# Optimization experiments

Hardware: AMD Instinct MI355X
Metric: run time of the kernel (lower is better)

Reference implementation:

```python
import jax, jax.numpy as jnp
import numpy as np

D_IN = 1024
D_OUT = 1024
NUM_HEADS = 16
HEAD_DIM = D_OUT // NUM_HEADS
WINDOW = 256


def setup_inputs() -> dict:
    key = jax.random.key(0)
    ks = jax.random.split(key, 6)
    s = 0.02
    x = jax.random.normal(ks[0], (2, 2048, D_IN), dtype=jnp.float32)
    Wq = jax.random.normal(ks[1], (D_IN, D_OUT), dtype=jnp.float32) * s
    Wk = jax.random.normal(ks[2], (D_IN, D_OUT), dtype=jnp.float32) * s
    Wv = jax.random.normal(ks[3], (D_IN, D_OUT), dtype=jnp.float32) * s
    Wo = jax.random.normal(ks[4], (D_OUT, D_OUT), dtype=jnp.float32) * s
    bo = jnp.zeros((D_OUT,), dtype=jnp.float32)
    return {"x": x, "Wq": Wq, "Wk": Wk, "Wv": Wv, "Wo": Wo, "bo": bo}


def reference(x, Wq, Wk, Wv, Wo, bo):
    b, s, _ = x.shape
    # project and split heads: [b, h, s, hd]
    def heads(t):
        return t.reshape(b, s, NUM_HEADS, HEAD_DIM).transpose(0, 2, 1, 3)
    q = heads(x @ Wq)
    k = heads(x @ Wk)
    v = heads(x @ Wv)
    scores = jnp.einsum('bhqd,bhkd->bhqk', q, k) / jnp.sqrt(jnp.float32(HEAD_DIM))
    # symmetric sliding-window band: |i - j| <= WINDOW
    i = jnp.arange(s)
    band = jnp.abs(i[:, None] - i[None, :]) <= WINDOW  # [s, s]
    scores = jnp.where(band[None, None], scores, -jnp.inf)
    probs = jax.nn.softmax(scores, axis=-1)  # dropout=0.0 -> identity
    ctx = jnp.einsum('bhqk,bhkd->bhqd', probs, v)
    ctx = ctx.transpose(0, 2, 1, 3).reshape(b, s, D_OUT)
    return ctx @ Wo + bo
```

## Files before the change

### kernel.cpp

```cpp
#include <hip/hip_runtime.h>
#include <hip/hip_bf16.h>

typedef __bf16 bf16_t;
typedef __bf16 bf16x8 __attribute__((ext_vector_type(8)));
typedef __bf16 bf16x4 __attribute__((ext_vector_type(4)));
typedef float  f32x4  __attribute__((ext_vector_type(4)));

#define SEQ    2048
#define BATCH  2
#define NHEAD  16
#define HDIM   64
#define DMODEL 1024
#define WIN    256

__device__ __forceinline__ void async_load16(const void* g, void* l) {
    __builtin_amdgcn_global_load_lds(
        (const __attribute__((address_space(1))) char*)(uintptr_t)g,
        (__attribute__((address_space(3))) char*)(uintptr_t)l, 16, 0, 0);
}

__global__ __launch_bounds__(256) void prep_kernel(
    const float* __restrict__ x, const float* __restrict__ Wq,
    const float* __restrict__ Wk, const float* __restrict__ Wv,
    const float* __restrict__ Wo, bf16_t* __restrict__ xb,
    bf16_t* __restrict__ Wt) {
    const int bid = blockIdx.x, tid = threadIdx.x;
    if (bid < 1024) {
        __shared__ float t64[64][65];
        const int mat = bid >> 8, tile = bid & 255;
        const int k0 = (tile >> 4) * 64, n0 = (tile & 15) * 64;
        const float* W = (mat == 0) ? Wq : (mat == 1) ? Wk : (mat == 2) ? Wv : Wo;
        bf16_t* out = Wt + (size_t)mat * DMODEL * DMODEL;
        const int r = tid >> 4, c4 = tid & 15;
#pragma unroll
        for (int i = 0; i < 4; i++) {
            int krow = i * 16 + r;
            float4 v = *(const float4*)&W[(size_t)(k0 + krow) * DMODEL + n0 + c4 * 4];
            t64[krow][c4 * 4 + 0] = v.x; t64[krow][c4 * 4 + 1] = v.y;
            t64[krow][c4 * 4 + 2] = v.z; t64[krow][c4 * 4 + 3] = v.w;
        }
        __syncthreads();
#pragma unroll
        for (int j = 0; j < 4; j++) {
            int nrow = j * 16 + r;
            bf16x4 o;
#pragma unroll
            for (int q = 0; q < 4; q++) o[q] = (bf16_t)t64[c4 * 4 + q][nrow];
            *(bf16x4*)&out[(size_t)(n0 + nrow) * DMODEL + k0 + c4 * 4] = o;
        }
    } else {
        const int cb = bid - 1024;
#pragma unroll
        for (int it = 0; it < 4; it++) {
            int i = (cb * 4 + it) * 256 + tid;
            float4 v = ((const float4*)x)[i];
            bf16x4 o;
            o[0] = (bf16_t)v.x; o[1] = (bf16_t)v.y; o[2] = (bf16_t)v.z; o[3] = (bf16_t)v.w;
            ((bf16x4*)xb)[i] = o;
        }
    }
}

__global__ __launch_bounds__(512) void gemm_qkv_kernel(
    const bf16_t* __restrict__ A, const bf16_t* __restrict__ Bt,
    bf16_t* __restrict__ Qb, bf16_t* __restrict__ Kb, bf16_t* __restrict__ Vt) {
    __shared__ __attribute__((aligned(16))) bf16_t smem[2][(256 + 192) * 64];
    const int tid = threadIdx.x;
    const int wave = tid >> 6, lane = tid & 63, quad = lane >> 4, l15 = lane & 15;
    const int wm = wave >> 2, wn = wave & 3;
    const int id = blockIdx.x, xcd = id & 7, tt = id >> 3;
    const int gidx = xcd * 32 + tt;
    const int m0 = (gidx & 15) * 256, n0 = (gidx >> 4) * 192;

    const int cth = (tid & 7) ^ ((tid >> 3) & 7);
    const int rA = tid >> 3;

    auto stage = [&](int tile, int buf) {
#pragma unroll
        for (int gr = 0; gr < 4; ++gr)
            async_load16(A + (size_t)(m0 + gr * 64 + rA) * 1024 + tile * 64 + cth * 8,
                         (char*)&smem[buf][0] + (size_t)(gr * 512 + tid) * 16);
#pragma unroll
        for (int gr = 0; gr < 3; ++gr)
            async_load16(Bt + (size_t)(n0 + gr * 64 + rA) * 1024 + tile * 64 + cth * 8,
                         (char*)&smem[buf][256 * 64] + (size_t)(gr * 512 + tid) * 16);
    };

    const int swz  = l15 & 7;
    const int rowA = wm * 128 + l15;
    const int rowB = wn * 48 + l15;

    f32x4 acc[8][3] = {};

    stage(0, 0);
    __syncthreads();
    int cur = 0;
#pragma unroll 1
    for (int t = 0; t < 16; ++t) {
        if (t + 1 < 16) stage(t + 1, cur ^ 1);
        const bf16_t* as = &smem[cur][0];
        const bf16_t* bs = &smem[cur][256 * 64];
#pragma unroll
        for (int kk = 0; kk < 2; ++kk) {
            const int chk = ((kk * 4 + quad) ^ swz) * 8;
            bf16x8 am[8], bn[3];
#pragma unroll
            for (int i = 0; i < 8; i++)
                am[i] = *(const bf16x8*)&as[(rowA + i * 16) * 64 + chk];
#pragma unroll
            for (int j = 0; j < 3; j++)
                bn[j] = *(const bf16x8*)&bs[(rowB + j * 16) * 64 + chk];
#pragma unroll
            for (int i = 0; i < 8; i++)
#pragma unroll
                for (int j = 0; j < 3; j++)
                    acc[i][j] = __builtin_amdgcn_mfma_f32_16x16x32_bf16(am[i], bn[j], acc[i][j], 0, 0, 0);
        }
        __syncthreads();
        cur ^= 1;
    }

#pragma unroll
    for (int i = 0; i < 8; i++)
#pragma unroll
        for (int j = 0; j < 3; j++) {
            const int mg0 = m0 + wm * 128 + i * 16 + quad * 4;
            const int ng  = n0 + wn * 48 + j * 16 + l15;
            const int sel = ng >> 10, nl = ng & 1023, h = nl >> 6, d = nl & 63;
            const int b = mg0 >> 11, s0 = mg0 & 2047;
            if (sel == 2) {
                bf16x4 o;
#pragma unroll
                for (int r = 0; r < 4; r++) o[r] = (bf16_t)acc[i][j][r];
                *(bf16x4*)&Vt[((size_t)((b * NHEAD + h) * HDIM + d)) * SEQ + s0] = o;
            } else {
#pragma unroll
                for (int r = 0; r < 4; r++) {
                    float v = acc[i][j][r];
                    size_t idx = ((size_t)((b * NHEAD + h) * SEQ) + s0 + r) * HDIM + d;
                    if (sel == 0) Qb[idx] = (bf16_t)(v * 0.18033688011112042f);
                    else          Kb[idx] = (bf16_t)v;
                }
            }
        }
}

__global__ __launch_bounds__(256) void gemm_out_kernel(
    const bf16_t* __restrict__ A, const bf16_t* __restrict__ Bt,
    float* __restrict__ Out, const float* __restrict__ bo) {
    __shared__ __attribute__((aligned(16))) bf16_t As[2][64 * 64];
    __shared__ __attribute__((aligned(16))) bf16_t Bs[2][128 * 64];
    const int tid = threadIdx.x;
    const int wn = tid >> 6, lane = tid & 63, quad = lane >> 4, l15 = lane & 15;
    const int id = blockIdx.x, xcd = id & 7, mt = id >> 3;
    const int m0 = mt * 64, n0 = xcd * 128;

    auto stage = [&](int kt, int buf) {
#pragma unroll
        for (int i = 0; i < 2; i++) {
            int v = tid + i * 256;
            int row = v >> 3, c = (v & 7) ^ (row & 7);
            async_load16(A + (size_t)(m0 + row) * 1024 + kt * 64 + c * 8,
                         (char*)&As[buf][0] + (size_t)v * 16);
        }
#pragma unroll
        for (int i = 0; i < 4; i++) {
            int v = tid + i * 256;
            int row = v >> 3, c = (v & 7) ^ (row & 7);
            async_load16(Bt + (size_t)(n0 + row) * 1024 + kt * 64 + c * 8,
                         (char*)&Bs[buf][0] + (size_t)v * 16);
        }
    };

    f32x4 acc[4][2] = {};
    stage(0, 0);
    __syncthreads();
    int cur = 0;
    for (int kt = 0; kt < 16; ++kt) {
        if (kt + 1 < 16) stage(kt + 1, cur ^ 1);
#pragma unroll
        for (int kk = 0; kk < 64; kk += 32) {
            bf16x8 am[4], bn[2];
#pragma unroll
            for (int i = 0; i < 4; i++) {
                int row = i * 16 + l15;
                int ch = ((kk >> 3) + quad) ^ (row & 7);
                am[i] = *(const bf16x8*)&As[cur][row * 64 + ch * 8];
            }
#pragma unroll
            for (int j = 0; j < 2; j++) {
                int row = wn * 32 + j * 16 + l15;
                int ch = ((kk >> 3) + quad) ^ (row & 7);
                bn[j] = *(const bf16x8*)&Bs[cur][row * 64 + ch * 8];
            }
#pragma unroll
            for (int i = 0; i < 4; i++)
#pragma unroll
                for (int j = 0; j < 2; j++)
                    acc[i][j] = __builtin_amdgcn_mfma_f32_16x16x32_bf16(am[i], bn[j], acc[i][j], 0, 0, 0);
        }
        __syncthreads();
        cur ^= 1;
    }

#pragma unroll
    for (int i = 0; i < 4; i++)
#pragma unroll
        for (int j = 0; j < 2; j++)
#pragma unroll
            for (int r = 0; r < 4; r++) {
                int mg = m0 + i * 16 + quad * 4 + r;
                int ng = n0 + wn * 32 + j * 16 + l15;
                Out[(size_t)mg * DMODEL + ng] = acc[i][j][r] + bo[ng];
            }
}

__global__ __launch_bounds__(512) void attn_kernel(
    const bf16_t* __restrict__ Qb, const bf16_t* __restrict__ Kb,
    const bf16_t* __restrict__ Vt, bf16_t* __restrict__ ctx) {
    __shared__ __attribute__((aligned(16))) bf16_t Ks[2][64 * 64];
    __shared__ __attribute__((aligned(16))) bf16_t Vs[2][64 * 64];
    __shared__ __attribute__((aligned(16))) bf16_t Plds[8][16][72];
    const int tid = threadIdx.x;
    const int wave = tid >> 6, lane = tid & 63, quad = lane >> 4, l15 = lane & 15;

    const int id = blockIdx.x;
    const int task = (id & 7) * 64 + (id >> 3);
    const int b = task >> 8, h = (task >> 4) & 15, Q0 = (task & 15) << 7;
    const int qbase = Q0 + wave * 16;
    const int wqt = (Q0 >> 6) + (wave >> 2);

    const bf16_t* Qp = Qb + (size_t)(b * NHEAD + h) * SEQ * HDIM;
    const bf16_t* Kp = Kb + (size_t)(b * NHEAD + h) * SEQ * HDIM;
    const bf16_t* Vp = Vt + (size_t)(b * NHEAD + h) * HDIM * SEQ;

    bf16x8 qa0 = *(const bf16x8*)(Qp + (size_t)(qbase + l15) * HDIM + quad * 8);
    bf16x8 qa1 = *(const bf16x8*)(Qp + (size_t)(qbase + l15) * HDIM + 32 + quad * 8);

    f32x4 O[4] = {};
    float psum = 0.0f;

    const int base_t = Q0 >> 6;
    const int bt0 = (base_t - 4 > 0) ? base_t - 4 : 0;
    const int bt1 = (base_t + 5 < SEQ / 64 - 1) ? base_t + 5 : SEQ / 64 - 1;

    auto stage = [&](int kt, int buf) {
        const int k0 = kt * 64;
        int v = tid;
        int row = v >> 3, c = (v & 7) ^ (row & 7);
        async_load16(Kp + (size_t)(k0 + row) * HDIM + c * 8, (char*)&Ks[buf][0] + (size_t)v * 16);
        async_load16(Vp + (size_t)row * SEQ + k0 + c * 8, (char*)&Vs[buf][0] + (size_t)v * 16);
    };

    stage(bt0, 0);
    int cb = 0;
    for (int kt = bt0; kt <= bt1; kt++) {
        __syncthreads();
        if (kt < bt1) stage(kt + 1, cb ^ 1);
        const int dt = kt - wqt;
        if (dt >= -4 && dt <= 4) {
            const int k0 = kt * 64;
            f32x4 st[4];
#pragma unroll
            for (int c = 0; c < 4; c++) {
                int row = c * 16 + l15;
                bf16x8 kb0 = *(const bf16x8*)&Ks[cb][row * 64 + (quad ^ (row & 7)) * 8];
                bf16x8 kb1 = *(const bf16x8*)&Ks[cb][row * 64 + ((quad + 4) ^ (row & 7)) * 8];
                f32x4 a = {};
                a = __builtin_amdgcn_mfma_f32_16x16x32_bf16(kb0, qa0, a, 0, 0, 0);
                a = __builtin_amdgcn_mfma_f32_16x16x32_bf16(kb1, qa1, a, 0, 0, 0);
                st[c] = a;
            }
            const bool edge = (dt == -4 || dt == 4);
            const int q = qbase + l15;
#pragma unroll
            for (int c = 0; c < 4; c++) {
                bf16x4 pk;
#pragma unroll
                for (int r = 0; r < 4; r++) {
                    float sv = st[c][r];
                    if (edge) {
                        int k = k0 + c * 16 + quad * 4 + r;
                        int dd = q - k; dd = (dd < 0) ? -dd : dd;
                        if (dd > WIN) sv = -1e30f;
                    }
                    pk[r] = (bf16_t)exp2f(sv);
                    psum += (float)pk[r];
                }
                *(bf16x4*)&Plds[wave][l15][c * 16 + quad * 4] = pk;
            }
            bf16x8 pa0 = *(const bf16x8*)&Plds[wave][l15][quad * 8];
            bf16x8 pa1 = *(const bf16x8*)&Plds[wave][l15][32 + quad * 8];
#pragma unroll
            for (int d = 0; d < 4; d++) {
                int row = d * 16 + l15;
                bf16x8 vb0 = *(const bf16x8*)&Vs[cb][row * 64 + (quad ^ (row & 7)) * 8];
                bf16x8 vb1 = *(const bf16x8*)&Vs[cb][row * 64 + ((quad + 4) ^ (row & 7)) * 8];
                O[d] = __builtin_amdgcn_mfma_f32_16x16x32_bf16(pa0, vb0, O[d], 0, 0, 0);
                O[d] = __builtin_amdgcn_mfma_f32_16x16x32_bf16(pa1, vb1, O[d], 0, 0, 0);
            }
        }
        cb ^= 1;
    }

    psum += __shfl_xor(psum, 16, 64);
    psum += __shfl_xor(psum, 32, 64);

#pragma unroll
    for (int r = 0; r < 4; r++) {
        float s_q = __shfl(psum, (quad << 4) | (quad * 4 + r), 64);
        float inv = 1.0f / s_q;
        int i = qbase + quad * 4 + r;
#pragma unroll
        for (int d = 0; d < 4; d++) {
            float v = O[d][r] * inv;
            ctx[((size_t)(b * SEQ + i)) * DMODEL + h * HDIM + d * 16 + l15] = (bf16_t)v;
        }
    }
}

extern "C" void kernel_launch(void* const* d_in, const int* in_sizes, int n_in,
                              void* d_out, int out_size, void* d_ws, size_t ws_size,
                              hipStream_t stream) {
    const float* x  = (const float*)d_in[0];
    const float* Wq = (const float*)d_in[1];
    const float* Wk = (const float*)d_in[2];
    const float* Wv = (const float*)d_in[3];
    const float* Wo = (const float*)d_in[4];
    const float* bo = (const float*)d_in[5];
    float* out = (float*)d_out;

    const size_t MTOK = (size_t)BATCH * SEQ;
    bf16_t* xb  = (bf16_t*)d_ws;
    bf16_t* Wt  = xb + MTOK * DMODEL;
    bf16_t* Qb  = Wt + (size_t)4 * DMODEL * DMODEL;
    bf16_t* Kb  = Qb + MTOK * DMODEL;
    bf16_t* Vt  = Kb + MTOK * DMODEL;
    bf16_t* ctx = Vt + MTOK * DMODEL;

    prep_kernel<<<dim3(2048), dim3(256), 0, stream>>>(x, Wq, Wk, Wv, Wo, xb, Wt);
    gemm_qkv_kernel<<<dim3(256), dim3(512), 0, stream>>>(xb, Wt, Qb, Kb, Vt);
    attn_kernel<<<dim3(512), dim3(512), 0, stream>>>(Qb, Kb, Vt, ctx);
    gemm_out_kernel<<<dim3(512), dim3(256), 0, stream>>>(
        ctx, Wt + (size_t)3 * DMODEL * DMODEL, out, bo);
}
```

Before: 156.9 us.

## Split attention KV range across wave halves with LDS merge of partial outputs

```diff
diff --git a/kernel.cpp b/kernel.cpp
--- a/kernel.cpp
+++ b/kernel.cpp
@@ -218,17 +218,22 @@
 __global__ __launch_bounds__(512) void attn_kernel(
     const bf16_t* __restrict__ Qb, const bf16_t* __restrict__ Kb,
     const bf16_t* __restrict__ Vt, bf16_t* __restrict__ ctx) {
-    __shared__ __attribute__((aligned(16))) bf16_t Ks[2][64 * 64];
-    __shared__ __attribute__((aligned(16))) bf16_t Vs[2][64 * 64];
-    __shared__ __attribute__((aligned(16))) bf16_t Plds[8][16][72];
+    __shared__ __attribute__((aligned(16))) char raw[51200];
+    bf16_t* Ks = (bf16_t*)&raw[0];
+    bf16_t* Vs = (bf16_t*)&raw[16384];
+    bf16_t (*Plds)[16][72] = (bf16_t(*)[16][72])&raw[32768];
+    float* Omrg = (float*)&raw[0];
+    float* Pmrg = (float*)&raw[16640];
+
     const int tid = threadIdx.x;
     const int wave = tid >> 6, lane = tid & 63, quad = lane >> 4, l15 = lane & 15;
+    const int p = wave & 3, half = wave >> 2;
 
     const int id = blockIdx.x;
-    const int task = (id & 7) * 64 + (id >> 3);
-    const int b = task >> 8, h = (task >> 4) & 15, Q0 = (task & 15) << 7;
-    const int qbase = Q0 + wave * 16;
-    const int wqt = (Q0 >> 6) + (wave >> 2);
+    const int task = (id & 7) * 128 + (id >> 3);
+    const int b = task >> 9, h = (task >> 5) & 15, Q0 = (task & 31) << 6;
+    const int qbase = Q0 + p * 16;
+    const int base_t = Q0 >> 6;
 
     const bf16_t* Qp = Qb + (size_t)(b * NHEAD + h) * SEQ * HDIM;
     const bf16_t* Kp = Kb + (size_t)(b * NHEAD + h) * SEQ * HDIM;
@@ -240,32 +245,37 @@
     f32x4 O[4] = {};
     float psum = 0.0f;
 
-    const int base_t = Q0 >> 6;
     const int bt0 = (base_t - 4 > 0) ? base_t - 4 : 0;
-    const int bt1 = (base_t + 5 < SEQ / 64 - 1) ? base_t + 5 : SEQ / 64 - 1;
+    const int bt1 = (base_t + 4 < SEQ / 64 - 1) ? base_t + 4 : SEQ / 64 - 1;
 
     auto stage = [&](int kt, int buf) {
         const int k0 = kt * 64;
         int v = tid;
         int row = v >> 3, c = (v & 7) ^ (row & 7);
-        async_load16(Kp + (size_t)(k0 + row) * HDIM + c * 8, (char*)&Ks[buf][0] + (size_t)v * 16);
-        async_load16(Vp + (size_t)row * SEQ + k0 + c * 8, (char*)&Vs[buf][0] + (size_t)v * 16);
+        async_load16(Kp + (size_t)(k0 + row) * HDIM + c * 8,
+                     (char*)&Ks[(size_t)buf * 4096] + (size_t)v * 16);
+        async_load16(Vp + (size_t)row * SEQ + k0 + c * 8,
+                     (char*)&Vs[(size_t)buf * 4096] + (size_t)v * 16);
     };
 
     stage(bt0, 0);
     int cb = 0;
+#pragma unroll 1
     for (int kt = bt0; kt <= bt1; kt++) {
         __syncthreads();
         if (kt < bt1) stage(kt + 1, cb ^ 1);
-        const int dt = kt - wqt;
-        if (dt >= -4 && dt <= 4) {
+        const int dt = kt - base_t;
+        const bool mine = half ? (dt >= 1 && dt <= 4) : (dt >= -4 && dt <= 0);
+        if (mine) {
             const int k0 = kt * 64;
+            const bf16_t* ks = &Ks[(size_t)cb * 4096];
+            const bf16_t* vs = &Vs[(size_t)cb * 4096];
             f32x4 st[4];
 #pragma unroll
             for (int c = 0; c < 4; c++) {
                 int row = c * 16 + l15;
-                bf16x8 kb0 = *(const bf16x8*)&Ks[cb][row * 64 + (quad ^ (row & 7)) * 8];
-                bf16x8 kb1 = *(const bf16x8*)&Ks[cb][row * 64 + ((quad + 4) ^ (row & 7)) * 8];
+                bf16x8 kb0 = *(const bf16x8*)&ks[row * 64 + (quad ^ (row & 7)) * 8];
+                bf16x8 kb1 = *(const bf16x8*)&ks[row * 64 + ((quad + 4) ^ (row & 7)) * 8];
                 f32x4 a = {};
                 a = __builtin_amdgcn_mfma_f32_16x16x32_bf16(kb0, qa0, a, 0, 0, 0);
                 a = __builtin_amdgcn_mfma_f32_16x16x32_bf16(kb1, qa1, a, 0, 0, 0);
@@ -294,8 +304,8 @@
 #pragma unroll
             for (int d = 0; d < 4; d++) {
                 int row = d * 16 + l15;
-                bf16x8 vb0 = *(const bf16x8*)&Vs[cb][row * 64 + (quad ^ (row & 7)) * 8];
-                bf16x8 vb1 = *(const bf16x8*)&Vs[cb][row * 64 + ((quad + 4) ^ (row & 7)) * 8];
+                bf16x8 vb0 = *(const bf16x8*)&vs[row * 64 + (quad ^ (row & 7)) * 8];
+                bf16x8 vb1 = *(const bf16x8*)&vs[row * 64 + ((quad + 4) ^ (row & 7)) * 8];
                 O[d] = __builtin_amdgcn_mfma_f32_16x16x32_bf16(pa0, vb0, O[d], 0, 0, 0);
                 O[d] = __builtin_amdgcn_mfma_f32_16x16x32_bf16(pa1, vb1, O[d], 0, 0, 0);
             }
@@ -303,18 +313,36 @@
         cb ^= 1;
     }
 
-    psum += __shfl_xor(psum, 16, 64);
-    psum += __shfl_xor(psum, 32, 64);
-
-#pragma unroll
-    for (int r = 0; r < 4; r++) {
-        float s_q = __shfl(psum, (quad << 4) | (quad * 4 + r), 64);
-        float inv = 1.0f / s_q;
-        int i = qbase + quad * 4 + r;
-#pragma unroll
-        for (int d = 0; d < 4; d++) {
-            float v = O[d][r] * inv;
-            ctx[((size_t)(b * SEQ + i)) * DMODEL + h * HDIM + d * 16 + l15] = (bf16_t)v;
+    __syncthreads();
+    if (half == 1) {
+#pragma unroll
+        for (int d = 0; d < 4; d++)
+#pragma unroll
+            for (int r = 0; r < 4; r++)
+                Omrg[(p * 16 + quad * 4 + r) * 65 + d * 16 + l15] = O[d][r];
+        Pmrg[p * 64 + lane] = psum;
+    }
+    __syncthreads();
+    if (half == 0) {
+        psum += Pmrg[p * 64 + lane];
+#pragma unroll
+        for (int d = 0; d < 4; d++)
+#pragma unroll
+            for (int r = 0; r < 4; r++)
+                O[d][r] += Omrg[(p * 16 + quad * 4 + r) * 65 + d * 16 + l15];
+
+        psum += __shfl_xor(psum, 16, 64);
+        psum += __shfl_xor(psum, 32, 64);
+#pragma unroll
+        for (int r = 0; r < 4; r++) {
+            float s_q = __shfl(psum, (quad << 4) | (quad * 4 + r), 64);
+            float inv = 1.0f / s_q;
+            int i = qbase + quad * 4 + r;
+#pragma unroll
+            for (int d = 0; d < 4; d++) {
+                float v = O[d][r] * inv;
+                ctx[((size_t)(b * SEQ + i)) * DMODEL + h * HDIM + d * 16 + l15] = (bf16_t)v;
+            }
         }
     }
 }
@@ -340,7 +368,7 @@
 
     prep_kernel<<<dim3(2048), dim3(256), 0, stream>>>(x, Wq, Wk, Wv, Wo, xb, Wt);
     gemm_qkv_kernel<<<dim3(256), dim3(512), 0, stream>>>(xb, Wt, Qb, Kb, Vt);
-    attn_kernel<<<dim3(512), dim3(512), 0, stream>>>(Qb, Kb, Vt, ctx);
+    attn_kernel<<<dim3(1024), dim3(512), 0, stream>>>(Qb, Kb, Vt, ctx);
     gemm_out_kernel<<<dim3(512), dim3(256), 0, stream>>>(
         ctx, Wt + (size_t)3 * DMODEL * DMODEL, out, bo);
 }
```

Result: slower. 161.4 us (+2.9%).
